# Optimization experiments

Hardware: AMD Instinct MI355X
Metric: run time of the kernel (lower is better)

Reference implementation:

```python
import jax, jax.numpy as jnp
import numpy as np

N = 100000      # nodes
E = 800000      # edges
IN1 = 128       # gcn input feature dim
IN2 = 64        # lstm input feature dim
H = 128         # hidden_channels
B = 32          # lstm batch
T = 200         # lstm seq len
OUT = 1         # out_channels
TARGET = jnp.array([0, 1000, 2000, 3000, 4000, 5000, 6000, 7000])  # numgcnE=8


def setup_inputs() -> dict:
    key = jax.random.key(0)
    ks = jax.random.split(key, 20)
    s = 0.05
    inp = {
        "data0": jax.random.normal(ks[0], (B, T, IN2), jnp.float32),
        "data1": jax.random.normal(ks[1], (N, IN1), jnp.float32),
        "edge_index": jax.random.randint(ks[2], (2, E), 0, N, dtype=jnp.int64),
        # GCNConv layers (weight stored [in, out])
        "W1": jax.random.normal(ks[3], (IN1, H), jnp.float32) * s,
        "b1": jnp.zeros((H,), jnp.float32),
        "W2": jax.random.normal(ks[4], (H, H), jnp.float32) * s,
        "b2": jnp.zeros((H,), jnp.float32),
        # LSTM1 (gate order i,f,g,o as in torch)
        "Wih1": jax.random.normal(ks[5], (4 * H, IN2), jnp.float32) * s,
        "Whh1": jax.random.normal(ks[6], (4 * H, H), jnp.float32) * s,
        "bih1": jnp.zeros((4 * H,), jnp.float32),
        "bhh1": jnp.zeros((4 * H,), jnp.float32),
        # LSTM2
        "Wih2": jax.random.normal(ks[7], (4 * H, H), jnp.float32) * s,
        "Whh2": jax.random.normal(ks[8], (4 * H, H), jnp.float32) * s,
        "bih2": jnp.zeros((4 * H,), jnp.float32),
        "bhh2": jnp.zeros((4 * H,), jnp.float32),
        # MLP head: (numgcnE+1)*H -> (numgcnE+1)*H/2 -> OUT
        "m1_w": jax.random.normal(ks[9], (9 * H, 9 * H // 2), jnp.float32) * s,
        "m1_b": jnp.zeros((9 * H // 2,), jnp.float32),
        "m2_w": jax.random.normal(ks[10], (9 * H // 2, OUT), jnp.float32) * s,
        "m2_b": jnp.zeros((OUT,), jnp.float32),
    }
    return inp


def gcn_conv(x, W, b, src, dst, n):
    # PyG GCNConv: self-loops + symmetric normalization, then scatter-add.
    xw = x @ W                                                     # [N, H]
    ones = jnp.ones(src.shape[0], xw.dtype)
    deg = jax.ops.segment_sum(ones, dst, num_segments=n) + 1.0     # +1 self-loop
    dinv = jax.lax.rsqrt(deg)                                      # [N]
    norm = dinv[src] * dinv[dst]                                   # [E]
    agg = jax.ops.segment_sum(xw[src] * norm[:, None], dst, num_segments=n)
    agg = agg + xw * (dinv * dinv)[:, None]                        # self-loop msgs
    return agg + b


def lstm_final(x_tbi, Wih, Whh, bih, bhh):
    # x_tbi: [T, Bsz, in]; returns final hidden state h_T [Bsz, H]
    Bsz = x_tbi.shape[1]
    Hh = Whh.shape[1]
    bias = bih + bhh

    def step(carry, xt):
        h, c = carry
        g = xt @ Wih.T + h @ Whh.T + bias                          # [Bsz, 4H]
        i, f, gg, o = jnp.split(g, 4, axis=-1)
        c = jax.nn.sigmoid(f) * c + jax.nn.sigmoid(i) * jnp.tanh(gg)
        h = jax.nn.sigmoid(o) * jnp.tanh(c)
        return (h, c), None

    init = (jnp.zeros((Bsz, Hh), x_tbi.dtype), jnp.zeros((Bsz, Hh), x_tbi.dtype))
    (h, c), _ = jax.lax.scan(step, init, x_tbi)
    return h


def reference(data0, data1, edge_index, W1, b1, W2, b2,
              Wih1, Whh1, bih1, bhh1, Wih2, Whh2, bih2, bhh2,
              m1_w, m1_b, m2_w, m2_b):
    src, dst = edge_index[0], edge_index[1]
    n = data1.shape[0]
    # two GCN layers with ReLU
    h = jax.nn.relu(gcn_conv(data1, W1, b1, src, dst, n))
    h = jax.nn.relu(gcn_conv(h, W2, b2, src, dst, n))
    g = h[TARGET].reshape(-1)                                      # [numgcnE*H]
    # lstm1 over [B, T, IN2] (batch_first) -> final h_n [B, H]
    h1 = lstm_final(jnp.swapaxes(data0, 0, 1), Wih1, Whh1, bih1, bhh1)
    # lstm2 consumes h_n[None] as [batch=1, seq=B, H] -> final h [1, H]
    h2 = lstm_final(h1[:, None, :], Wih2, Whh2, bih2, bhh2)[0]     # [H]
    d = jnp.concatenate([g, h2])                                   # [(numgcnE+1)*H]
    return (d @ m1_w + m1_b) @ m2_w + m2_b                         # [OUT]
```

## Files before the change

kernel.cpp:

```cpp
#include <hip/hip_runtime.h>
#include <hip/hip_bf16.h>
#include <cstring>

using bf16 = __hip_bfloat16;
typedef _Float16 h2v __attribute__((ext_vector_type(2)));
typedef _Float16 h8v __attribute__((ext_vector_type(8)));

#if __has_builtin(__builtin_amdgcn_fdot2)
__device__ __forceinline__ float FDOT2(h2v a, h2v b, float c) {
    return __builtin_amdgcn_fdot2(a, b, c, false);
}
#else
__device__ __forceinline__ float FDOT2(h2v a, h2v b, float c) {
    return c + (float)a.x * (float)b.x + (float)a.y * (float)b.y;
}
#endif

__device__ __forceinline__ float sigm_f(float x) {
    return __builtin_amdgcn_rcpf(1.f + __expf(-x));
}
__device__ __forceinline__ float tanh_f(float x) {
    return 1.f - 2.f * __builtin_amdgcn_rcpf(1.f + __expf(2.f * x));
}

constexpr int NH    = 128;
constexpr int G4    = 512;
constexpr int TSEQ  = 200;
constexpr int BBATCH= 32;
constexpr int NTGT  = 8;

constexpr int LCAP1 = 1024;
constexpr int S1CAP = LCAP1 + NTGT;
constexpr int LCAP2 = 8192;
constexpr int S2CAP = LCAP2 + S1CAP;

constexpr size_t algn(size_t x) { return (x + 255) & ~size_t(255); }
constexpr size_t OFF_GX1  = 0;
constexpr size_t OFF_GX2  = algn(OFF_GX1  + 6400ull * G4 * 4);
constexpr size_t OFF_DEG  = algn(OFF_GX2  + 32ull * G4 * 4);
constexpr size_t OFF_DINV = algn(OFF_DEG  + 100000ull * 4);
constexpr size_t OFF_SL1  = algn(OFF_DINV + 100000ull * 4);
constexpr size_t OFF_SL2  = algn(OFF_SL1  + 100000ull * 4);
constexpr size_t OFF_CNT  = algn(OFF_SL2  + 100000ull * 4);
constexpr size_t OFF_L1   = algn(OFF_CNT  + 64);
constexpr size_t OFF_S1   = algn(OFF_L1   + (size_t)LCAP1 * 8);
constexpr size_t OFF_L2   = algn(OFF_S1   + (size_t)S1CAP * 4);
constexpr size_t OFF_S2   = algn(OFF_L2   + (size_t)LCAP2 * 8);
constexpr size_t OFF_XW1  = algn(OFF_S2   + (size_t)S2CAP * 4);
constexpr size_t OFF_H1   = algn(OFF_XW1  + (size_t)S2CAP * NH * 4);
constexpr size_t OFF_XW2  = algn(OFF_H1   + (size_t)S1CAP * NH * 4);
constexpr size_t OFF_DVEC = algn(OFF_XW2  + (size_t)S1CAP * NH * 4);
constexpr size_t OFF_H1F  = algn(OFF_DVEC + 1152ull * 4);
constexpr size_t OFF_CACC = algn(OFF_H1F  + 32ull * NH * 4);
constexpr size_t WS_NEEDED = OFF_CACC + 576ull * 4;

__device__ __forceinline__ int edge_at(const int* ei, int E, int is64, int row, int e) {
    return is64 ? ei[(((size_t)row * E) + e) * 2] : ei[((size_t)row * E) + e];
}

__device__ __forceinline__ float dinv_of(const int* deg, int v) {
    return rsqrtf((float)deg[v] + 1.0f);
}

__global__ void k_canary(unsigned int* out, unsigned int bits) {
    if (threadIdx.x == 0) out[0] = bits;
}


__global__ void k_init(const int* ei, int* deg, int* slot1, int* slot2, int* cnt,
                       float* colacc, int n) {
    int i = blockIdx.x * 256 + threadIdx.x;
    if (i < 14) cnt[i] = 0;
    if (i == 15) cnt[15] = (ei[1] == 0 && ei[3] == 0 && ei[5] == 0 && ei[7] == 0) ? 1 : 0;
    if (i < 576) colacc[i] = 0.f;
    for (; i < n; i += gridDim.x * 256) { deg[i] = 0; slot1[i] = -1; slot2[i] = -1; }
}

__global__ void k_deg_l1(const int* ei, int E, int* deg, int2* l1, int* cnt) {
    int is64 = cnt[15];
    for (int e = blockIdx.x * 256 + threadIdx.x; e < E; e += gridDim.x * 256) {
        int d = edge_at(ei, E, is64, 1, e);
        if ((unsigned)d < 100000u) atomicAdd(&deg[d], 1);
        if (d <= 7000 && d >= 0 && d % 1000 == 0) {
            int s = edge_at(ei, E, is64, 0, e);
            int idx = atomicAdd(&cnt[0], 1);
            if (idx < LCAP1) l1[idx] = make_int2(s, d);
        }
    }
}

__global__ void k_s1(const int2* l1, int* cnt, int* slot1, int* s1list,
                     int* slot2, int* s2list) {
    __shared__ int ns1;
    if (threadIdx.x == 0) ns1 = 0;
    __syncthreads();
    int m = min(cnt[0], LCAP1);
    for (int i = threadIdx.x; i < NTGT + m; i += blockDim.x) {
        int v = (i < NTGT) ? i * 1000 : l1[i - NTGT].x;
        if ((unsigned)v >= 100000u) continue;
        int old = atomicCAS(&slot1[v], -1, -2);
        if (old == -1) {
            int idx = atomicAdd(&ns1, 1);
            if (idx < S1CAP) { s1list[idx] = v; atomicExch(&slot1[v], idx); }
        }
    }
    __syncthreads();
    int n1 = min(ns1, S1CAP);
    if (threadIdx.x == 0) cnt[1] = n1;
    for (int i = threadIdx.x; i < n1; i += blockDim.x) {
        int v = s1list[i];
        int old = atomicCAS(&slot2[v], -1, -2);
        if (old == -1) {
            int idx = atomicAdd(&cnt[2], 1);
            if (idx < S2CAP) { s2list[idx] = v; atomicExch(&slot2[v], idx); }
        }
    }
}

__global__ void k_l2(const int* ei, int E, const int* slot1,
                     int2* l2, int* cnt, int* slot2, int* s2list) {
    int is64 = cnt[15];
    for (int e = blockIdx.x * 256 + threadIdx.x; e < E; e += gridDim.x * 256) {
        int d = edge_at(ei, E, is64, 1, e);
        if ((unsigned)d >= 100000u) continue;
        if (slot1[d] >= 0) {
            int s = edge_at(ei, E, is64, 0, e);
            if ((unsigned)s >= 100000u) continue;
            int idx = atomicAdd(&cnt[3], 1);
            if (idx < LCAP2) l2[idx] = make_int2(s, d);
            int old = atomicCAS(&slot2[s], -1, -2);
            if (old == -1) {
                int j = atomicAdd(&cnt[2], 1);
                if (j < S2CAP) { s2list[j] = s; atomicExch(&slot2[s], j); }
            }
        }
    }
}


__global__ void k_xw1(const float* x, const float* W, const int* s2list, const int* cnt, float* xw1) {
    int i = blockIdx.x;
    if (i >= min(cnt[2], S2CAP)) return;
    int node = s2list[i];
    __shared__ float xs[NH];
    int c = threadIdx.x;
    xs[c] = x[(size_t)node * NH + c];
    __syncthreads();
    float acc = 0.f;
    #pragma unroll 8
    for (int k = 0; k < NH; k++) acc += xs[k] * W[(size_t)k * NH + c];
    xw1[(size_t)i * NH + c] = acc;
}

__global__ void k_h1init(const float* xw1, const int* s1list, const int* cnt,
                         const int* slot2, const int* deg, float* h1) {
    int i = blockIdx.x;
    if (i >= min(cnt[1], S1CAP)) return;
    int node = s1list[i];
    int s2 = slot2[node];
    if (s2 < 0 || s2 >= S2CAP) s2 = 0;
    float v = dinv_of(deg, node);
    h1[i * NH + threadIdx.x] = xw1[(size_t)s2 * NH + threadIdx.x] * v * v;
}

__global__ void k_h1scat(const float* xw1, const int2* l2, const int* cnt,
                         const int* slot1, const int* slot2, const int* deg, float* h1) {
    int e = blockIdx.x;
    if (e >= min(cnt[3], LCAP2)) return;
    int2 sd = l2[e];
    int t1 = slot1[sd.y], s2 = slot2[sd.x];
    if (t1 < 0 || t1 >= S1CAP || s2 < 0 || s2 >= S2CAP) return;
    float w = dinv_of(deg, sd.x) * dinv_of(deg, sd.y);
    atomicAdd(&h1[t1 * NH + threadIdx.x],
              xw1[(size_t)s2 * NH + threadIdx.x] * w);
}

__global__ void k_xw2(const float* h1, const float* W, const float* b1, const int* cnt, float* xw2) {
    int i = blockIdx.x;
    if (i >= min(cnt[1], S1CAP)) return;
    __shared__ float xs[NH];
    int c = threadIdx.x;
    xs[c] = fmaxf(h1[i * NH + c] + b1[c], 0.f);
    __syncthreads();
    float acc = 0.f;
    #pragma unroll 8
    for (int k = 0; k < NH; k++) acc += xs[k] * W[(size_t)k * NH + c];
    xw2[(size_t)i * NH + c] = acc;
}

__global__ void k_gout(const float* xw2, const int2* l1, const int* cnt,
                       const int* slot1, const int* deg, const float* b2, float* dvec) {
    int t = blockIdx.x;
    int tgt = t * 1000;
    int c = threadIdx.x;
    float vt = dinv_of(deg, tgt);
    int st = slot1[tgt]; if (st < 0 || st >= S1CAP) st = 0;
    float acc = xw2[(size_t)st * NH + c] * vt * vt;
    int m = min(cnt[0], LCAP1);
    for (int e = 0; e < m; e++) {
        int2 sd = l1[e];
        if (sd.y == tgt) {
            int ss = slot1[sd.x];
            if (ss >= 0 && ss < S1CAP)
                acc += xw2[(size_t)ss * NH + c] * dinv_of(deg, sd.x) * vt;
        }
    }
    acc += b2[c];
    dvec[t * NH + c] = fmaxf(acc, 0.f);
}


__global__ __launch_bounds__(256) void k_gx1(const float* data0, const float* Wih,
                                             const float* bih, const float* bhh, float* gx) {
    constexpr int LDP = 68;
    __shared__ float As[64 * LDP];
    __shared__ float Bs[64 * LDP];
    int tid = threadIdx.x;
    int rb = blockIdx.x >> 3;
    int gb = blockIdx.x & 7;
    int r0 = rb * 64, g0 = gb * 64;
    for (int i = tid; i < 64 * 64; i += 256) {
        int rr = i >> 6, k = i & 63;
        int r = r0 + rr, b = r & 31, t = r >> 5;
        As[rr * LDP + k] = data0[((size_t)b * TSEQ + t) * 64 + k];
        Bs[rr * LDP + k] = Wih[(size_t)(g0 + rr) * 64 + k];
    }
    __syncthreads();
    int tr = (tid & 15) * 4;
    int tg = (tid >> 4) * 4;
    float acc[4][4] = {};
    #pragma unroll
    for (int k4 = 0; k4 < 16; k4++) {
        float4 a0 = *(const float4*)&As[(tr + 0) * LDP + k4 * 4];
        float4 a1 = *(const float4*)&As[(tr + 1) * LDP + k4 * 4];
        float4 a2 = *(const float4*)&As[(tr + 2) * LDP + k4 * 4];
        float4 a3 = *(const float4*)&As[(tr + 3) * LDP + k4 * 4];
        float4 b0 = *(const float4*)&Bs[(tg + 0) * LDP + k4 * 4];
        float4 b1 = *(const float4*)&Bs[(tg + 1) * LDP + k4 * 4];
        float4 b2 = *(const float4*)&Bs[(tg + 2) * LDP + k4 * 4];
        float4 b3 = *(const float4*)&Bs[(tg + 3) * LDP + k4 * 4];
        const float4 av[4] = {a0, a1, a2, a3};
        const float4 bv[4] = {b0, b1, b2, b3};
        #pragma unroll
        for (int i = 0; i < 4; i++)
            #pragma unroll
            for (int j = 0; j < 4; j++)
                acc[i][j] += av[i].x * bv[j].x + av[i].y * bv[j].y
                           + av[i].z * bv[j].z + av[i].w * bv[j].w;
    }
    float bias[4];
    #pragma unroll
    for (int j = 0; j < 4; j++) bias[j] = bih[g0 + tg + j] + bhh[g0 + tg + j];
    #pragma unroll
    for (int i = 0; i < 4; i++) {
        size_t row = (size_t)(r0 + tr + i) * G4 + g0 + tg;
        #pragma unroll
        for (int j = 0; j < 4; j++) gx[row + j] = acc[i][j] + bias[j];
    }
}

__global__ void k_gx2(const float* h1f, const float* Wih,
                      const float* bih, const float* bhh, float* gx) {
    int t = blockIdx.x;
    __shared__ float xs[NH];
    int tid = threadIdx.x;
    int g0 = tid, g1 = tid + 256;
    if (tid < NH) xs[tid] = h1f[t * NH + tid];
    __syncthreads();
    float a0 = bih[g0] + bhh[g0];
    float a1 = bih[g1] + bhh[g1];
    #pragma unroll 4
    for (int k = 0; k < NH; k++) {
        a0 += Wih[(size_t)g0 * NH + k] * xs[k];
        a1 += Wih[(size_t)g1 * NH + k] * xs[k];
    }
    gx[(size_t)t * G4 + g0] = a0;
    gx[(size_t)t * G4 + g1] = a1;
}

template<int T, int NB>
__global__ __launch_bounds__(256, 1) void k_lstm(const float* gx, const float* Whh, float* hfinal) {
    int b = blockIdx.x;
    int tid = threadIdx.x;
    int w = tid >> 6, l = tid & 63;
    int j = w * 32 + (l & 31);
    int role = l >> 5;
    int r0 = role ? (j + NH) : j;
    int r1 = role ? (j + 3 * NH) : (j + 2 * NH);
    __shared__ __align__(16) _Float16 hbuf[2][NH];
    h2v w0[NH / 2], w1[NH / 2];
    #pragma unroll
    for (int k = 0; k < NH; k += 4) {
        float4 a = *(const float4*)&Whh[(size_t)r0 * NH + k];
        w0[k / 2]     = h2v{(_Float16)a.x, (_Float16)a.y};
        w0[k / 2 + 1] = h2v{(_Float16)a.z, (_Float16)a.w};
        float4 c4 = *(const float4*)&Whh[(size_t)r1 * NH + k];
        w1[k / 2]     = h2v{(_Float16)c4.x, (_Float16)c4.y};
        w1[k / 2 + 1] = h2v{(_Float16)c4.z, (_Float16)c4.w};
    }
    if (tid < NH) { hbuf[0][tid] = (_Float16)0.f; hbuf[1][tid] = (_Float16)0.f; }
    float c = 0.f, hout = 0.f;
    float nx0 = gx[((size_t)0 * NB + b) * G4 + r0];
    float nx1 = gx[((size_t)0 * NB + b) * G4 + r1];
    __syncthreads();
    for (int t = 0; t < T; t++) {
        const h8v* hv8 = (const h8v*)hbuf[t & 1];
        float a0 = nx0, a1 = nx1;
        int tn = (t + 1 < T) ? (t + 1) : t;
        nx0 = gx[((size_t)tn * NB + b) * G4 + r0];
        nx1 = gx[((size_t)tn * NB + b) * G4 + r1];
        float p0 = 0.f, q0 = 0.f, p1 = 0.f, q1 = 0.f;
        #pragma unroll
        for (int m = 0; m < NH / 8; m++) {
            h8v h8 = hv8[m];
            h2v ha = __builtin_shufflevector(h8, h8, 0, 1);
            h2v hb = __builtin_shufflevector(h8, h8, 2, 3);
            h2v hc = __builtin_shufflevector(h8, h8, 4, 5);
            h2v hd = __builtin_shufflevector(h8, h8, 6, 7);
            p0 = FDOT2(w0[4 * m],     ha, p0);
            q0 = FDOT2(w0[4 * m + 1], hb, q0);
            p0 = FDOT2(w0[4 * m + 2], hc, p0);
            q0 = FDOT2(w0[4 * m + 3], hd, q0);
            p1 = FDOT2(w1[4 * m],     ha, p1);
            q1 = FDOT2(w1[4 * m + 1], hb, q1);
            p1 = FDOT2(w1[4 * m + 2], hc, p1);
            q1 = FDOT2(w1[4 * m + 3], hd, q1);
        }
        float ga = a0 + p0 + q0;
        float gb = a1 + p1 + q1;
        float s  = sigm_f(ga);
        float tg = role ? sigm_f(gb) : tanh_f(gb);
        float u  = s * tg;
        float fv = __shfl_xor(s,  32);
        float ov = __shfl_xor(tg, 32);
        if (role == 0) {
            c = fv * c + u;
            hout = ov * tanh_f(c);
            hbuf[(t + 1) & 1][j] = (_Float16)hout;
        }
        __syncthreads();
    }
    if (role == 0) hfinal[(size_t)b * NH + j] = hout;
}

__global__ __launch_bounds__(64) void k_head1(const float* dvec, const float* m1w, float* colacc) {
    int rg = blockIdx.x & 7;
    int cg = blockIdx.x >> 3;
    int col = cg * 64 + threadIdx.x;
    int r0 = rg * 144;
    float acc = 0.f;
    #pragma unroll 4
    for (int i = r0; i < r0 + 144; i++)
        acc += dvec[i] * m1w[(size_t)i * 576 + col];
    atomicAdd(&colacc[col], acc);
}

__global__ __launch_bounds__(256) void k_head2(const float* colacc, const float* m1b,
                                               const float* m2w, const float* m2b,
                                               unsigned int* out) {
    __shared__ float wr[4];
    int j = threadIdx.x;
    float sum = 0.f;
    for (int col = j; col < 576; col += 256)
        sum += (colacc[col] + m1b[col]) * m2w[col];
    #pragma unroll
    for (int off = 32; off > 0; off >>= 1) sum += __shfl_down(sum, off, 64);
    if ((j & 63) == 0) wr[j >> 6] = sum;
    __syncthreads();
    if (j == 0) {
        float s = wr[0] + wr[1] + wr[2] + wr[3] + m2b[0];
        bf16 hb = __float2bfloat16(s);
        unsigned short u;
        memcpy(&u, &hb, 2);
        out[0] = ((unsigned int)u << 16) | u;
    }
}


extern "C" void kernel_launch(void* const* d_in, const int* in_sizes, int n_in,
                              void* d_out, int out_size, void* d_ws, size_t ws_size,
                              hipStream_t stream) {
    const float* data0 = (const float*)d_in[0];
    const float* data1 = (const float*)d_in[1];
    const int*   ei    = (const int*)d_in[2];
    const float* W1    = (const float*)d_in[3];
    const float* b1    = (const float*)d_in[4];
    const float* W2    = (const float*)d_in[5];
    const float* b2    = (const float*)d_in[6];
    const float* Wih1  = (const float*)d_in[7];
    const float* Whh1  = (const float*)d_in[8];
    const float* bih1  = (const float*)d_in[9];
    const float* bhh1  = (const float*)d_in[10];
    const float* Wih2  = (const float*)d_in[11];
    const float* Whh2  = (const float*)d_in[12];
    const float* bih2  = (const float*)d_in[13];
    const float* bhh2  = (const float*)d_in[14];
    const float* m1w   = (const float*)d_in[15];
    const float* m1b   = (const float*)d_in[16];
    const float* m2w   = (const float*)d_in[17];
    const float* m2b   = (const float*)d_in[18];

    const int n = in_sizes[1] / NH;
    const int E = in_sizes[2] / 2;

    char* ws = (char*)d_ws;
    float* gx1   = (float*)(ws + OFF_GX1);
    float* gx2   = (float*)(ws + OFF_GX2);
    int*   deg   = (int*)  (ws + OFF_DEG);
    int*   slot1 = (int*)  (ws + OFF_SL1);
    int*   slot2 = (int*)  (ws + OFF_SL2);
    int*   cnt   = (int*)  (ws + OFF_CNT);
    int2*  l1    = (int2*) (ws + OFF_L1);
    int*   s1l   = (int*)  (ws + OFF_S1);
    int2*  l2    = (int2*) (ws + OFF_L2);
    int*   s2l   = (int*)  (ws + OFF_S2);
    float* xw1   = (float*)(ws + OFF_XW1);
    float* h1    = (float*)(ws + OFF_H1);
    float* xw2   = (float*)(ws + OFF_XW2);
    float* dvec  = (float*)(ws + OFF_DVEC);
    float* h1f   = (float*)(ws + OFF_H1F);
    float* cacc  = (float*)(ws + OFF_CACC);

    float v = 1.0f + (ws_size < WS_NEEDED ? 1.0f : 0.0f) + (n_in != 19 ? 2.0f : 0.0f);
    unsigned int fb; memcpy(&fb, &v, 4);
    unsigned int hi = fb >> 16;
    unsigned int canary_bits = (hi << 16) | hi;
    k_canary <<<1, 64, 0, stream>>>((unsigned int*)d_out, canary_bits);

    int nb = (n + 255) / 256;
    int eb = (E + 255) / 256;

    k_init   <<<nb, 256, 0, stream>>>(ei, deg, slot1, slot2, cnt, cacc, n);
    k_deg_l1 <<<eb, 256, 0, stream>>>(ei, E, deg, l1, cnt);
    k_s1     <<<1, 256, 0, stream>>>(l1, cnt, slot1, s1l, slot2, s2l);
    k_l2     <<<eb, 256, 0, stream>>>(ei, E, slot1, l2, cnt, slot2, s2l);
    k_xw1    <<<S2CAP, NH, 0, stream>>>(data1, W1, s2l, cnt, xw1);
    k_h1init <<<S1CAP, NH, 0, stream>>>(xw1, s1l, cnt, slot2, deg, h1);
    k_h1scat <<<LCAP2, NH, 0, stream>>>(xw1, l2, cnt, slot1, slot2, deg, h1);
    k_xw2    <<<S1CAP, NH, 0, stream>>>(h1, W2, b1, cnt, xw2);
    k_gout   <<<NTGT, NH, 0, stream>>>(xw2, l1, cnt, slot1, deg, b2, dvec);
    k_gx1    <<<800, 256, 0, stream>>>(data0, Wih1, bih1, bhh1, gx1);
    k_lstm<TSEQ, BBATCH><<<BBATCH, 256, 0, stream>>>(gx1, Whh1, h1f);
    k_gx2    <<<BBATCH, 256, 0, stream>>>(h1f, Wih2, bih2, bhh2, gx2);
    k_lstm<BBATCH, 1>  <<<1, 256, 0, stream>>>(gx2, Whh2, dvec + 1024);
    k_head1  <<<72, 64, 0, stream>>>(dvec, m1w, cacc);
    k_head2  <<<1, 256, 0, stream>>>(cacc, m1b, m2w, m2b, (unsigned int*)d_out);
    (void)out_size;
}
```

Measured before the change: 403.3 us.

## Fuse canary/h1init into other kernels and restructure LSTM to one thread per hidden unit

Drops the canary kernel by writing its value in k_init, and drops k_h1init by zeroing h1 in k_init and folding the self-loop term into k_xw2, which removes two launches. The LSTM kernel moves from 256 threads with paired gate roles and a cross-lane shuffle to 128 threads, each computing all four gates for one hidden unit. This removes the shuffle and halves the block size, but doubles per-thread register weights (256 h2v values) and the serial FDOT2 chain per step, which may lengthen each recurrent step. That matters because the 200-step LSTM likely dominates the kernel time.

After: 588.6 us. 45.9% more time.

```diff
diff --git a/kernel.cpp b/kernel.cpp
--- a/kernel.cpp
+++ b/kernel.cpp
@@ -62,18 +62,16 @@
     return rsqrtf((float)deg[v] + 1.0f);
 }
 
-__global__ void k_canary(unsigned int* out, unsigned int bits) {
-    if (threadIdx.x == 0) out[0] = bits;
-}
-
-
 __global__ void k_init(const int* ei, int* deg, int* slot1, int* slot2, int* cnt,
-                       float* colacc, int n) {
-    int i = blockIdx.x * 256 + threadIdx.x;
-    if (i < 14) cnt[i] = 0;
-    if (i == 15) cnt[15] = (ei[1] == 0 && ei[3] == 0 && ei[5] == 0 && ei[7] == 0) ? 1 : 0;
-    if (i < 576) colacc[i] = 0.f;
-    for (; i < n; i += gridDim.x * 256) { deg[i] = 0; slot1[i] = -1; slot2[i] = -1; }
+                       float* h1, float* colacc, int n, unsigned int* out, unsigned int canary) {
+    int i0 = blockIdx.x * 256 + threadIdx.x;
+    int gstride = gridDim.x * 256;
+    if (i0 < 14) cnt[i0] = 0;
+    if (i0 == 15) cnt[15] = (ei[1] == 0 && ei[3] == 0 && ei[5] == 0 && ei[7] == 0) ? 1 : 0;
+    if (i0 == 16) out[0] = canary;
+    if (i0 < 576) colacc[i0] = 0.f;
+    for (int i = i0; i < S1CAP * NH; i += gstride) h1[i] = 0.f;
+    for (int i = i0; i < n; i += gstride) { deg[i] = 0; slot1[i] = -1; slot2[i] = -1; }
 }
 
 __global__ void k_deg_l1(const int* ei, int E, int* deg, int2* l1, int* cnt) {
@@ -152,17 +150,6 @@
     xw1[(size_t)i * NH + c] = acc;
 }
 
-__global__ void k_h1init(const float* xw1, const int* s1list, const int* cnt,
-                         const int* slot2, const int* deg, float* h1) {
-    int i = blockIdx.x;
-    if (i >= min(cnt[1], S1CAP)) return;
-    int node = s1list[i];
-    int s2 = slot2[node];
-    if (s2 < 0 || s2 >= S2CAP) s2 = 0;
-    float v = dinv_of(deg, node);
-    h1[i * NH + threadIdx.x] = xw1[(size_t)s2 * NH + threadIdx.x] * v * v;
-}
-
 __global__ void k_h1scat(const float* xw1, const int2* l2, const int* cnt,
                          const int* slot1, const int* slot2, const int* deg, float* h1) {
     int e = blockIdx.x;
@@ -175,12 +162,18 @@
               xw1[(size_t)s2 * NH + threadIdx.x] * w);
 }
 
-__global__ void k_xw2(const float* h1, const float* W, const float* b1, const int* cnt, float* xw2) {
+__global__ void k_xw2(const float* h1, const float* xw1, const float* W, const float* b1,
+                      const int* cnt, const int* s1list, const int* slot2, const int* deg,
+                      float* xw2) {
     int i = blockIdx.x;
     if (i >= min(cnt[1], S1CAP)) return;
     __shared__ float xs[NH];
     int c = threadIdx.x;
-    xs[c] = fmaxf(h1[i * NH + c] + b1[c], 0.f);
+    int node = s1list[i];
+    int s2i = slot2[node];
+    if (s2i < 0 || s2i >= S2CAP) s2i = 0;
+    float v = dinv_of(deg, node);
+    xs[c] = fmaxf(h1[i * NH + c] + xw1[(size_t)s2i * NH + c] * (v * v) + b1[c], 0.f);
     __syncthreads();
     float acc = 0.f;
     #pragma unroll 8
@@ -279,37 +272,41 @@
 }
 
 template<int T, int NB>
-__global__ __launch_bounds__(256, 1) void k_lstm(const float* gx, const float* Whh, float* hfinal) {
+__global__ __launch_bounds__(128, 1) void k_lstm(const float* gx, const float* Whh, float* hfinal) {
     int b = blockIdx.x;
     int tid = threadIdx.x;
-    int w = tid >> 6, l = tid & 63;
-    int j = w * 32 + (l & 31);
-    int role = l >> 5;
-    int r0 = role ? (j + NH) : j;
-    int r1 = role ? (j + 3 * NH) : (j + 2 * NH);
+    int j = tid;
     __shared__ __align__(16) _Float16 hbuf[2][NH];
-    h2v w0[NH / 2], w1[NH / 2];
+    h2v w0[NH / 2], w1[NH / 2], w2[NH / 2], w3[NH / 2];
     #pragma unroll
     for (int k = 0; k < NH; k += 4) {
-        float4 a = *(const float4*)&Whh[(size_t)r0 * NH + k];
-        w0[k / 2]     = h2v{(_Float16)a.x, (_Float16)a.y};
-        w0[k / 2 + 1] = h2v{(_Float16)a.z, (_Float16)a.w};
-        float4 c4 = *(const float4*)&Whh[(size_t)r1 * NH + k];
-        w1[k / 2]     = h2v{(_Float16)c4.x, (_Float16)c4.y};
-        w1[k / 2 + 1] = h2v{(_Float16)c4.z, (_Float16)c4.w};
-    }
-    if (tid < NH) { hbuf[0][tid] = (_Float16)0.f; hbuf[1][tid] = (_Float16)0.f; }
+        float4 ai = *(const float4*)&Whh[(size_t)j * NH + k];
+        w0[k / 2]     = h2v{(_Float16)ai.x, (_Float16)ai.y};
+        w0[k / 2 + 1] = h2v{(_Float16)ai.z, (_Float16)ai.w};
+        float4 af = *(const float4*)&Whh[(size_t)(j + NH) * NH + k];
+        w1[k / 2]     = h2v{(_Float16)af.x, (_Float16)af.y};
+        w1[k / 2 + 1] = h2v{(_Float16)af.z, (_Float16)af.w};
+        float4 ag = *(const float4*)&Whh[(size_t)(j + 2 * NH) * NH + k];
+        w2[k / 2]     = h2v{(_Float16)ag.x, (_Float16)ag.y};
+        w2[k / 2 + 1] = h2v{(_Float16)ag.z, (_Float16)ag.w};
+        float4 ao = *(const float4*)&Whh[(size_t)(j + 3 * NH) * NH + k];
+        w3[k / 2]     = h2v{(_Float16)ao.x, (_Float16)ao.y};
+        w3[k / 2 + 1] = h2v{(_Float16)ao.z, (_Float16)ao.w};
+    }
+    hbuf[0][tid] = (_Float16)0.f;
+    hbuf[1][tid] = (_Float16)0.f;
     float c = 0.f, hout = 0.f;
-    float nx0 = gx[((size_t)0 * NB + b) * G4 + r0];
-    float nx1 = gx[((size_t)0 * NB + b) * G4 + r1];
+    const float* g0p = &gx[(size_t)b * G4];
+    float nx0 = g0p[j], nx1 = g0p[j + NH], nx2 = g0p[j + 2 * NH], nx3 = g0p[j + 3 * NH];
     __syncthreads();
     for (int t = 0; t < T; t++) {
         const h8v* hv8 = (const h8v*)hbuf[t & 1];
-        float a0 = nx0, a1 = nx1;
+        float a0 = nx0, a1 = nx1, a2 = nx2, a3 = nx3;
         int tn = (t + 1 < T) ? (t + 1) : t;
-        nx0 = gx[((size_t)tn * NB + b) * G4 + r0];
-        nx1 = gx[((size_t)tn * NB + b) * G4 + r1];
+        const float* gp = &gx[((size_t)tn * NB + b) * G4];
+        nx0 = gp[j]; nx1 = gp[j + NH]; nx2 = gp[j + 2 * NH]; nx3 = gp[j + 3 * NH];
         float p0 = 0.f, q0 = 0.f, p1 = 0.f, q1 = 0.f;
+        float p2 = 0.f, q2 = 0.f, p3 = 0.f, q3 = 0.f;
         #pragma unroll
         for (int m = 0; m < NH / 8; m++) {
             h8v h8 = hv8[m];
@@ -325,22 +322,29 @@
             q1 = FDOT2(w1[4 * m + 1], hb, q1);
             p1 = FDOT2(w1[4 * m + 2], hc, p1);
             q1 = FDOT2(w1[4 * m + 3], hd, q1);
-        }
-        float ga = a0 + p0 + q0;
-        float gb = a1 + p1 + q1;
-        float s  = sigm_f(ga);
-        float tg = role ? sigm_f(gb) : tanh_f(gb);
-        float u  = s * tg;
-        float fv = __shfl_xor(s,  32);
-        float ov = __shfl_xor(tg, 32);
-        if (role == 0) {
-            c = fv * c + u;
-            hout = ov * tanh_f(c);
-            hbuf[(t + 1) & 1][j] = (_Float16)hout;
-        }
+            p2 = FDOT2(w2[4 * m],     ha, p2);
+            q2 = FDOT2(w2[4 * m + 1], hb, q2);
+            p2 = FDOT2(w2[4 * m + 2], hc, p2);
+            q2 = FDOT2(w2[4 * m + 3], hd, q2);
+            p3 = FDOT2(w3[4 * m],     ha, p3);
+            q3 = FDOT2(w3[4 * m + 1], hb, q3);
+            p3 = FDOT2(w3[4 * m + 2], hc, p3);
+            q3 = FDOT2(w3[4 * m + 3], hd, q3);
+        }
+        float gi = a0 + p0 + q0;
+        float gf = a1 + p1 + q1;
+        float gg = a2 + p2 + q2;
+        float go = a3 + p3 + q3;
+        float si = sigm_f(gi);
+        float sf = sigm_f(gf);
+        float tg = tanh_f(gg);
+        float so = sigm_f(go);
+        c = sf * c + si * tg;
+        hout = so * tanh_f(c);
+        hbuf[(t + 1) & 1][j] = (_Float16)hout;
         __syncthreads();
     }
-    if (role == 0) hfinal[(size_t)b * NH + j] = hout;
+    hfinal[(size_t)b * NH + j] = hout;
 }
 
 __global__ __launch_bounds__(64) void k_head1(const float* dvec, const float* m1w, float* colacc) {
@@ -425,24 +429,23 @@
     unsigned int fb; memcpy(&fb, &v, 4);
     unsigned int hi = fb >> 16;
     unsigned int canary_bits = (hi << 16) | hi;
-    k_canary <<<1, 64, 0, stream>>>((unsigned int*)d_out, canary_bits);
 
     int nb = (n + 255) / 256;
     int eb = (E + 255) / 256;
 
-    k_init   <<<nb, 256, 0, stream>>>(ei, deg, slot1, slot2, cnt, cacc, n);
+    k_init   <<<nb, 256, 0, stream>>>(ei, deg, slot1, slot2, cnt, h1, cacc, n,
+                                      (unsigned int*)d_out, canary_bits);
     k_deg_l1 <<<eb, 256, 0, stream>>>(ei, E, deg, l1, cnt);
     k_s1     <<<1, 256, 0, stream>>>(l1, cnt, slot1, s1l, slot2, s2l);
     k_l2     <<<eb, 256, 0, stream>>>(ei, E, slot1, l2, cnt, slot2, s2l);
     k_xw1    <<<S2CAP, NH, 0, stream>>>(data1, W1, s2l, cnt, xw1);
-    k_h1init <<<S1CAP, NH, 0, stream>>>(xw1, s1l, cnt, slot2, deg, h1);
     k_h1scat <<<LCAP2, NH, 0, stream>>>(xw1, l2, cnt, slot1, slot2, deg, h1);
-    k_xw2    <<<S1CAP, NH, 0, stream>>>(h1, W2, b1, cnt, xw2);
+    k_xw2    <<<S1CAP, NH, 0, stream>>>(h1, xw1, W2, b1, cnt, s1l, slot2, deg, xw2);
     k_gout   <<<NTGT, NH, 0, stream>>>(xw2, l1, cnt, slot1, deg, b2, dvec);
     k_gx1    <<<800, 256, 0, stream>>>(data0, Wih1, bih1, bhh1, gx1);
-    k_lstm<TSEQ, BBATCH><<<BBATCH, 256, 0, stream>>>(gx1, Whh1, h1f);
+    k_lstm<TSEQ, BBATCH><<<BBATCH, 128, 0, stream>>>(gx1, Whh1, h1f);
     k_gx2    <<<BBATCH, 256, 0, stream>>>(h1f, Wih2, bih2, bhh2, gx2);
-    k_lstm<BBATCH, 1>  <<<1, 256, 0, stream>>>(gx2, Whh2, dvec + 1024);
+    k_lstm<BBATCH, 1>  <<<1, 128, 0, stream>>>(gx2, Whh2, dvec + 1024);
     k_head1  <<<72, 64, 0, stream>>>(dvec, m1w, cacc);
     k_head2  <<<1, 256, 0, stream>>>(cacc, m1b, m2w, m2b, (unsigned int*)d_out);
     (void)out_size;
```
